# Kernel tuning notes

Hardware: AMD Instinct MI355X
Metric: run time of the kernel (lower is better)

## Reference

```python
import jax, jax.numpy as jnp
import numpy as np

NCLS, NDF, B = 256, 512, 1024
ALP = 0.1


def setup_inputs() -> dict:
    key = jax.random.key(0)
    k1, k2, k3 = jax.random.split(key, 3)
    df = jax.random.normal(k1, (B, NDF), dtype=jnp.float32)
    gt = jax.random.randint(k2, (B,), 0, NCLS)
    fc = jax.random.normal(k3, (NCLS, NDF), dtype=jnp.float32)
    return {"df": df, "gt": gt, "fc": fc}


def _update_stats(df, gt):
    """Sequential per-sample running mean/var update (moving_avg=False branch).
    Faithful to the torch no_grad loop: per-class counter `it`, c1=it/(it+1),
    c2=1/(it+1); mean[t]=f when it==0 else mean[t]*c1+f*c2;
    var[t]=var[t]*c1 + (f-mean[t])**2 * c1*c2. Buffers start at zero.
    """
    mean0 = jnp.zeros((NCLS, NDF), jnp.float32)
    var0 = jnp.zeros((NCLS, NDF), jnp.float32)
    it0 = jnp.zeros((NCLS,), jnp.int32)

    def step(carry, xt):
        mean, var, it = carry
        f, t = xt
        n = it[t]
        nf = n.astype(jnp.float32)
        c1 = nf / (nf + 1.0)
        c2 = 1.0 / (nf + 1.0)
        m_t = jnp.where(n == 0, f, mean[t] * c1 + f * c2)
        a = (f - m_t) ** 2
        v_t = var[t] * c1 + a * c1 * c2
        return (mean.at[t].set(m_t), var.at[t].set(v_t), it.at[t].add(1)), None

    (mean, var, it), _ = jax.lax.scan(step, (mean0, var0, it0), (df, gt))
    return mean, var


def reference(df, gt, fc):
    # stats updated from detached features (torch uses no_grad)
    _, var = _update_stats(jax.lax.stop_gradient(df), gt)
    Var = var[gt]          # (B, ndf)
    Fc = fc[gt]            # (B, ndf): column of fc for each sample's class
    W = fc[None, :, :] - Fc[:, None, :]  # (B, ncls, ndf)
    # score[b,c] = W[b,c,:].df[b,:] + alp/2 * (W**2)[b,c,:].Var[b,:]
    score = jnp.einsum('bcd,bd->bc', W, df) \
        + 0.5 * ALP * jnp.einsum('bcd,bd->bc', W * W, Var)
    return score[:, :, None]  # (B, ncls, 1), matching torch matmul output
```

## Files before the change

### kernel.cpp

```cpp
#include <hip/hip_runtime.h>

#define NCLS 256
#define NDF  512
#define BSZ  1024
#define ALP  0.1f


typedef __attribute__((ext_vector_type(8))) short bf16x8;
typedef __attribute__((ext_vector_type(4))) float f32x4;

__device__ __forceinline__ unsigned rne_pk(float lo, float hi) {
    union { float f; unsigned u; } a, b;
    a.f = lo; b.f = hi;
    unsigned ua = (a.u + 0x7FFFu + ((a.u >> 16) & 1u)) >> 16;
    unsigned ub = (b.u + 0x7FFFu + ((b.u >> 16) & 1u)) & 0xFFFF0000u;
    return ua | ub;
}
__device__ __forceinline__ uint4 pk16(float4 p, float4 q) {
    uint4 r;
    r.x = rne_pk(p.x, p.y); r.y = rne_pk(p.z, p.w);
    r.z = rne_pk(q.x, q.y); r.w = rne_pk(q.z, q.w);
    return r;
}
__device__ __forceinline__ float bf16r(float x) {
    union { float f; unsigned u; } c; c.f = x;
    c.u = (c.u + 0x7FFFu + ((c.u >> 16) & 1u)) & 0xFFFF0000u;
    return c.f;
}

__global__ __launch_bounds__(512) void k1_R_bias(const float* __restrict__ df,
                                                 const int* __restrict__ gt,
                                                 const float* __restrict__ fc,
                                                 float* __restrict__ Rp,
                                                 float* __restrict__ bias1) {
    __shared__ union {
        struct { alignas(16) char A[64 * 256]; alignas(16) char B[64 * 256]; } g;
        struct { int gts[BSZ]; unsigned long long bmap[64 * 16]; } r;
    } sm;

    const int tid = threadIdx.x;
    const int bid = blockIdx.x;
    const int lane = tid & 63;
    const int wv = tid >> 6;

    for (int i = tid; i < BSZ; i += 512) sm.r.gts[i] = gt[i];
    for (int i = tid; i < 1024; i += 512) sm.r.bmap[i] = 0ull;
    __syncthreads();
    for (int i = tid; i < BSZ; i += 512) {
        const int c = sm.r.gts[i] - ((bid >> 3) & 3) * 64;
        if ((unsigned)c < 64u) atomicOr(&sm.r.bmap[c * 16 + (i >> 6)], 1ull << (i & 63));
    }

    const int z = bid & 7;
    const int tile = bid >> 3;
    const int bm = tile & 3, bn = tile >> 2;
    const int D0 = z * 64;
    const int sr = tid >> 2;
    const int sswz = (sr & 7) << 4;
    const int clocal = sr;
    const int myclass = bm * 64 + (clocal & 63);
    const int dim0 = D0 + (tid & 3) * 16;
    const int kbl = (tid & 3) * 32;
    const int kbq = 128 + kbl;

    float fcq[16];
    float4 b0, b1, b2, b3;
    int bsample = 0, bt = 0;
    if (wv < 4) {
        const float* Bg = fc + (bn * 64 + sr) * NDF + dim0;
        b0 = ((const float4*)Bg)[0]; b1 = ((const float4*)Bg)[1];
        b2 = ((const float4*)Bg)[2]; b3 = ((const float4*)Bg)[3];
        const float* fct = fc + myclass * NDF + dim0;
        const float4 q0 = ((const float4*)fct)[0], q1 = ((const float4*)fct)[1];
        const float4 q2 = ((const float4*)fct)[2], q3 = ((const float4*)fct)[3];
        fcq[0]=q0.x; fcq[1]=q0.y; fcq[2]=q0.z; fcq[3]=q0.w;
        fcq[4]=q1.x; fcq[5]=q1.y; fcq[6]=q1.z; fcq[7]=q1.w;
        fcq[8]=q2.x; fcq[9]=q2.y; fcq[10]=q2.z; fcq[11]=q2.w;
        fcq[12]=q3.x; fcq[13]=q3.y; fcq[14]=q3.z; fcq[15]=q3.w;
    } else {
        bsample = bid * 8 + (wv - 4) * 2 + (lane >> 5);
        bt = sm.r.gts[bsample];
    }
    __syncthreads();

    float m[16], v[16];
    if (wv < 4) {
#pragma unroll
        for (int j = 0; j < 16; ++j) { m[j] = 0.f; v[j] = 0.f; }
        float nf = 0.f;
        int w = 0;
        unsigned long long bits = sm.r.bmap[clocal * 16];
        auto next = [&]() -> int {
            while (bits == 0ull) {
                if (w >= 15) return -1;
                bits = sm.r.bmap[clocal * 16 + (++w)];
            }
            const int b = __ffsll((unsigned long long)bits) - 1;
            bits &= bits - 1ull;
            return (w << 6) + b;
        };
        int cur = next();
        float f[16];
        if (cur >= 0) {
            const float* p = df + cur * NDF + dim0;
            const float4 q0 = ((const float4*)p)[0], q1 = ((const float4*)p)[1];
            const float4 q2 = ((const float4*)p)[2], q3 = ((const float4*)p)[3];
            f[0]=q0.x; f[1]=q0.y; f[2]=q0.z; f[3]=q0.w;
            f[4]=q1.x; f[5]=q1.y; f[6]=q1.z; f[7]=q1.w;
            f[8]=q2.x; f[9]=q2.y; f[10]=q2.z; f[11]=q2.w;
            f[12]=q3.x; f[13]=q3.y; f[14]=q3.z; f[15]=q3.w;
        }
        while (cur >= 0) {
            const int nxt = next();
            float g[16];
            if (nxt >= 0) {
                const float* p = df + nxt * NDF + dim0;
                const float4 q0 = ((const float4*)p)[0], q1 = ((const float4*)p)[1];
                const float4 q2 = ((const float4*)p)[2], q3 = ((const float4*)p)[3];
                g[0]=q0.x; g[1]=q0.y; g[2]=q0.z; g[3]=q0.w;
                g[4]=q1.x; g[5]=q1.y; g[6]=q1.z; g[7]=q1.w;
                g[8]=q2.x; g[9]=q2.y; g[10]=q2.z; g[11]=q2.w;
                g[12]=q3.x; g[13]=q3.y; g[14]=q3.z; g[15]=q3.w;
            }
            const float c2 = 1.0f / (nf + 1.0f);
            const float c1 = nf * c2;
            const float c12 = c1 * c2;
#pragma unroll
            for (int j = 0; j < 16; ++j) {
                m[j] = m[j] * c1 + f[j] * c2;
                const float a = f[j] - m[j];
                v[j] = v[j] * c1 + a * a * c12;
            }
            nf += 1.0f;
#pragma unroll
            for (int j = 0; j < 16; ++j) f[j] = g[j];
            cur = nxt;
        }
    } else {
        const int l32 = lane & 31;
        const float* pd = df + bsample * NDF + l32 * 16;
        const float* pf = fc + bt * NDF + l32 * 16;
        float s = 0.f;
#pragma unroll
        for (int i = 0; i < 4; ++i) {
            const float4 dq = ((const float4*)pd)[i];
            const float4 fq = ((const float4*)pf)[i];
            s = fmaf(bf16r(dq.x), bf16r(fq.x), s);
            s = fmaf(bf16r(dq.y), bf16r(fq.y), s);
            s = fmaf(bf16r(dq.z), bf16r(fq.z), s);
            s = fmaf(bf16r(dq.w), bf16r(fq.w), s);
        }
        s += __shfl_xor(s, 1); s += __shfl_xor(s, 2); s += __shfl_xor(s, 4);
        s += __shfl_xor(s, 8); s += __shfl_xor(s, 16);
        if (l32 == 0) bias1[bsample] = s;
    }
    __syncthreads();

    if (wv < 4) {
        char* arow = sm.g.A + sr * 256;
        char* brow = sm.g.B + sr * 256;
        float4 l0, l1, l2, l3;
        l0.x=-2.f*fcq[0]*v[0];  l0.y=-2.f*fcq[1]*v[1];  l0.z=-2.f*fcq[2]*v[2];  l0.w=-2.f*fcq[3]*v[3];
        l1.x=-2.f*fcq[4]*v[4];  l1.y=-2.f*fcq[5]*v[5];  l1.z=-2.f*fcq[6]*v[6];  l1.w=-2.f*fcq[7]*v[7];
        l2.x=-2.f*fcq[8]*v[8];  l2.y=-2.f*fcq[9]*v[9];  l2.z=-2.f*fcq[10]*v[10]; l2.w=-2.f*fcq[11]*v[11];
        l3.x=-2.f*fcq[12]*v[12]; l3.y=-2.f*fcq[13]*v[13]; l3.z=-2.f*fcq[14]*v[14]; l3.w=-2.f*fcq[15]*v[15];
        float4 p0, p1, p2, p3;
        p0.x=v[0];  p0.y=v[1];  p0.z=v[2];  p0.w=v[3];
        p1.x=v[4];  p1.y=v[5];  p1.z=v[6];  p1.w=v[7];
        p2.x=v[8];  p2.y=v[9];  p2.z=v[10]; p2.w=v[11];
        p3.x=v[12]; p3.y=v[13]; p3.z=v[14]; p3.w=v[15];
        float4 s0, s1, s2, s3;
        s0.x=b0.x*b0.x; s0.y=b0.y*b0.y; s0.z=b0.z*b0.z; s0.w=b0.w*b0.w;
        s1.x=b1.x*b1.x; s1.y=b1.y*b1.y; s1.z=b1.z*b1.z; s1.w=b1.w*b1.w;
        s2.x=b2.x*b2.x; s2.y=b2.y*b2.y; s2.z=b2.z*b2.z; s2.w=b2.w*b2.w;
        s3.x=b3.x*b3.x; s3.y=b3.y*b3.y; s3.z=b3.z*b3.z; s3.w=b3.w*b3.w;
        *(uint4*)(arow + ((kbl + 0) ^ sswz)) = pk16(l0, l1);
        *(uint4*)(arow + ((kbl + 16) ^ sswz)) = pk16(l2, l3);
        *(uint4*)(arow + ((kbq + 0) ^ sswz)) = pk16(p0, p1);
        *(uint4*)(arow + ((kbq + 16) ^ sswz)) = pk16(p2, p3);
        *(uint4*)(brow + ((kbl + 0) ^ sswz)) = pk16(b0, b1);
        *(uint4*)(brow + ((kbl + 16) ^ sswz)) = pk16(b2, b3);
        *(uint4*)(brow + ((kbq + 0) ^ sswz)) = pk16(s0, s1);
        *(uint4*)(brow + ((kbq + 16) ^ sswz)) = pk16(s2, s3);
    }
    __syncthreads();

    if (wv < 4) {
        const int fr = lane & 15;
        const int fkb = (lane >> 4) * 16;
        const int fswz = (fr & 7) << 4;
        const int wm = (wv >> 1) * 32, wn = (wv & 1) * 32;
        f32x4 acc[2][2];
        acc[0][0] = 0.f; acc[0][1] = 0.f; acc[1][0] = 0.f; acc[1][1] = 0.f;
#pragma unroll
        for (int st = 0; st < 4; ++st) {
            const int kb = (st * 64 + fkb) ^ fswz;
            const bf16x8 aF0 = *(const bf16x8*)(sm.g.A + (wm + fr) * 256 + kb);
            const bf16x8 aF1 = *(const bf16x8*)(sm.g.A + (wm + 16 + fr) * 256 + kb);
            const bf16x8 bF0 = *(const bf16x8*)(sm.g.B + (wn + fr) * 256 + kb);
            const bf16x8 bF1 = *(const bf16x8*)(sm.g.B + (wn + 16 + fr) * 256 + kb);
            acc[0][0] = __builtin_amdgcn_mfma_f32_16x16x32_bf16(aF0, bF0, acc[0][0], 0, 0, 0);
            acc[0][1] = __builtin_amdgcn_mfma_f32_16x16x32_bf16(aF0, bF1, acc[0][1], 0, 0, 0);
            acc[1][0] = __builtin_amdgcn_mfma_f32_16x16x32_bf16(aF1, bF0, acc[1][0], 0, 0, 0);
            acc[1][1] = __builtin_amdgcn_mfma_f32_16x16x32_bf16(aF1, bF1, acc[1][1], 0, 0, 0);
        }
        float* base = Rp + z * (NCLS * NCLS) + (bm * 64) * NCLS + bn * 64;
#pragma unroll
        for (int mi = 0; mi < 2; ++mi)
#pragma unroll
            for (int ni = 0; ni < 2; ++ni)
#pragma unroll
                for (int r2 = 0; r2 < 4; ++r2)
                    base[(wm + mi * 16 + (lane >> 4) * 4 + r2) * NCLS + wn + ni * 16 + fr] =
                        acc[mi][ni][r2];
    }
}

__global__ __launch_bounds__(512) void k2_s1_out(const float* __restrict__ df,
                                                 const int* __restrict__ gt,
                                                 const float* __restrict__ fc,
                                                 const float* __restrict__ Rp,
                                                 const float* __restrict__ bias1,
                                                 float* __restrict__ out) {
    __shared__ union {
        struct { alignas(16) char A[32 * 1024]; alignas(16) char B[32 * 1024]; } t;
        float fold[8 * 256];
    } sm;

    const int tid = threadIdx.x;
    const int bn = blockIdx.x & 7, bm = blockIdx.x >> 3;
    const int lane = tid & 63, wv = tid >> 6;

    const int row = tid >> 4, seg = tid & 15;
    const float* Ag = df + (bm * 32 + row) * NDF + seg * 32;
    const float* Bg = fc + (bn * 32 + row) * NDF + seg * 32;
    float4 a[8], b[8];
#pragma unroll
    for (int i = 0; i < 8; ++i) a[i] = ((const float4*)Ag)[i];
#pragma unroll
    for (int i = 0; i < 8; ++i) b[i] = ((const float4*)Bg)[i];
    const int swz = (row & 7) << 4;
    char* ar = sm.t.A + row * 1024;
    char* br = sm.t.B + row * 1024;
#pragma unroll
    for (int j = 0; j < 4; ++j)
        *(uint4*)(ar + ((seg * 64 + j * 16) ^ swz)) = pk16(a[2 * j], a[2 * j + 1]);
#pragma unroll
    for (int j = 0; j < 4; ++j)
        *(uint4*)(br + ((seg * 64 + j * 16) ^ swz)) = pk16(b[2 * j], b[2 * j + 1]);
    __syncthreads();

    const int q = wv & 3, h = wv >> 2;
    const int wm = (q >> 1) * 16, wn = (q & 1) * 16;
    const int fr = lane & 15;
    const int fkb = (lane >> 4) * 16;
    const int fswz = (fr & 7) << 4;
    f32x4 acc = 0.f;
#pragma unroll
    for (int s = 0; s < 8; ++s) {
        const int kb = ((h * 8 + s) * 64 + fkb) ^ fswz;
        const bf16x8 aF = *(const bf16x8*)(sm.t.A + (wm + fr) * 1024 + kb);
        const bf16x8 bF = *(const bf16x8*)(sm.t.B + (wn + fr) * 1024 + kb);
        acc = __builtin_amdgcn_mfma_f32_16x16x32_bf16(aF, bF, acc, 0, 0, 0);
    }
    __syncthreads();
    ((f32x4*)sm.fold)[wv * 64 + lane] = acc;
    __syncthreads();
    const f32x4 other = ((f32x4*)sm.fold)[(wv ^ 4) * 64 + lane];
    acc += other;

    const int colg = bn * 32 + wn + fr;
#pragma unroll
    for (int rr = 0; rr < 2; ++rr) {
        const float av = h ? ((rr == 0) ? acc[2] : acc[3])
                           : ((rr == 0) ? acc[0] : acc[1]);
        const int r = h * 2 + rr;
        const int bg = bm * 32 + wm + (lane >> 4) * 4 + r;
        const int t = gt[bg];
        float vR = 0.f, vtt = 0.f;
#pragma unroll
        for (int z = 0; z < 8; ++z) {
            const float* rp = Rp + z * (NCLS * NCLS) + t * NCLS;
            vR += rp[colg];
            vtt += rp[t];
        }
        out[bg * NCLS + colg] = (av - bias1[bg]) + 0.5f * ALP * (vR - vtt);
    }
}

extern "C" void kernel_launch(void* const* d_in, const int* in_sizes, int n_in,
                              void* d_out, int out_size, void* d_ws, size_t ws_size,
                              hipStream_t stream) {
    const float* df = (const float*)d_in[0];
    const int* gt = (const int*)d_in[1];
    const float* fc = (const float*)d_in[2];
    float* out = (float*)d_out;

    float* ws = (float*)d_ws;
    float* Rp = ws;
    float* bias1 = Rp + 8 * NCLS * NCLS;

    k1_R_bias<<<128, 512, 0, stream>>>(df, gt, fc, Rp, bias1);
    k2_s1_out<<<256, 512, 0, stream>>>(df, gt, fc, Rp, bias1, out);
}
```

Measured before the change: 25.34 us.

## Load MFMA fragments directly from global in k2, drop LDS staging and K-split

The second kernel no longer stages df/fc tiles through swizzled LDS. Each lane now loads its bf16 fragments straight from global memory and packs them in registers. The K-split across two wave halves, with its LDS fold and barriers, is replaced by 4 waves that each cover the full K using two interleaved accumulators, and the block size drops from 512 to 256 threads. This removes LDS traffic and three syncthreads, but each element is now loaded redundantly by the waves sharing a row or column, and each wave runs a longer serial MFMA chain.

```diff
diff --git a/kernel.cpp b/kernel.cpp
--- a/kernel.cpp
+++ b/kernel.cpp
@@ -21,6 +21,9 @@
     r.x = rne_pk(p.x, p.y); r.y = rne_pk(p.z, p.w);
     r.z = rne_pk(q.x, q.y); r.w = rne_pk(q.z, q.w);
     return r;
+}
+__device__ __forceinline__ bf16x8 pkfrag(float4 p, float4 q) {
+    return __builtin_bit_cast(bf16x8, pk16(p, q));
 }
 __device__ __forceinline__ float bf16r(float x) {
     union { float f; unsigned u; } c; c.f = x;
@@ -216,65 +219,40 @@
     }
 }
 
-__global__ __launch_bounds__(512) void k2_s1_out(const float* __restrict__ df,
+__global__ __launch_bounds__(256) void k2_s1_out(const float* __restrict__ df,
                                                  const int* __restrict__ gt,
                                                  const float* __restrict__ fc,
                                                  const float* __restrict__ Rp,
                                                  const float* __restrict__ bias1,
                                                  float* __restrict__ out) {
-    __shared__ union {
-        struct { alignas(16) char A[32 * 1024]; alignas(16) char B[32 * 1024]; } t;
-        float fold[8 * 256];
-    } sm;
-
     const int tid = threadIdx.x;
     const int bn = blockIdx.x & 7, bm = blockIdx.x >> 3;
     const int lane = tid & 63, wv = tid >> 6;
-
-    const int row = tid >> 4, seg = tid & 15;
-    const float* Ag = df + (bm * 32 + row) * NDF + seg * 32;
-    const float* Bg = fc + (bn * 32 + row) * NDF + seg * 32;
-    float4 a[8], b[8];
-#pragma unroll
-    for (int i = 0; i < 8; ++i) a[i] = ((const float4*)Ag)[i];
-#pragma unroll
-    for (int i = 0; i < 8; ++i) b[i] = ((const float4*)Bg)[i];
-    const int swz = (row & 7) << 4;
-    char* ar = sm.t.A + row * 1024;
-    char* br = sm.t.B + row * 1024;
-#pragma unroll
-    for (int j = 0; j < 4; ++j)
-        *(uint4*)(ar + ((seg * 64 + j * 16) ^ swz)) = pk16(a[2 * j], a[2 * j + 1]);
-#pragma unroll
-    for (int j = 0; j < 4; ++j)
-        *(uint4*)(br + ((seg * 64 + j * 16) ^ swz)) = pk16(b[2 * j], b[2 * j + 1]);
-    __syncthreads();
-
-    const int q = wv & 3, h = wv >> 2;
-    const int wm = (q >> 1) * 16, wn = (q & 1) * 16;
+    const int wm = (wv >> 1) * 16, wn = (wv & 1) * 16;
     const int fr = lane & 15;
-    const int fkb = (lane >> 4) * 16;
-    const int fswz = (fr & 7) << 4;
-    f32x4 acc = 0.f;
-#pragma unroll
-    for (int s = 0; s < 8; ++s) {
-        const int kb = ((h * 8 + s) * 64 + fkb) ^ fswz;
-        const bf16x8 aF = *(const bf16x8*)(sm.t.A + (wm + fr) * 1024 + kb);
-        const bf16x8 bF = *(const bf16x8*)(sm.t.B + (wn + fr) * 1024 + kb);
-        acc = __builtin_amdgcn_mfma_f32_16x16x32_bf16(aF, bF, acc, 0, 0, 0);
-    }
-    __syncthreads();
-    ((f32x4*)sm.fold)[wv * 64 + lane] = acc;
-    __syncthreads();
-    const f32x4 other = ((f32x4*)sm.fold)[(wv ^ 4) * 64 + lane];
-    acc += other;
+    const int ksub = (lane >> 4) * 8;
+
+    const float* Arow = df + (bm * 32 + wm + fr) * NDF + ksub;
+    const float* Brow = fc + (bn * 32 + wn + fr) * NDF + ksub;
+
+    f32x4 accE = 0.f, accO = 0.f;
+#pragma unroll
+    for (int s = 0; s < 16; s += 2) {
+        const float4 a00 = ((const float4*)(Arow + s * 32))[0];
+        const float4 a01 = ((const float4*)(Arow + s * 32))[1];
+        const float4 b00 = ((const float4*)(Brow + s * 32))[0];
+        const float4 b01 = ((const float4*)(Brow + s * 32))[1];
+        const float4 a10 = ((const float4*)(Arow + s * 32 + 32))[0];
+        const float4 a11 = ((const float4*)(Arow + s * 32 + 32))[1];
+        const float4 b10 = ((const float4*)(Brow + s * 32 + 32))[0];
+        const float4 b11 = ((const float4*)(Brow + s * 32 + 32))[1];
+        accE = __builtin_amdgcn_mfma_f32_16x16x32_bf16(pkfrag(a00, a01), pkfrag(b00, b01), accE, 0, 0, 0);
+        accO = __builtin_amdgcn_mfma_f32_16x16x32_bf16(pkfrag(a10, a11), pkfrag(b10, b11), accO, 0, 0, 0);
+    }
 
     const int colg = bn * 32 + wn + fr;
 #pragma unroll
-    for (int rr = 0; rr < 2; ++rr) {
-        const float av = h ? ((rr == 0) ? acc[2] : acc[3])
-                           : ((rr == 0) ? acc[0] : acc[1]);
-        const int r = h * 2 + rr;
+    for (int r = 0; r < 4; ++r) {
         const int bg = bm * 32 + wm + (lane >> 4) * 4 + r;
         const int t = gt[bg];
         float vR = 0.f, vtt = 0.f;
@@ -284,7 +262,8 @@
             vR += rp[colg];
             vtt += rp[t];
         }
-        out[bg * NCLS + colg] = (av - bias1[bg]) + 0.5f * ALP * (vR - vtt);
+        out[bg * NCLS + colg] = (accE[r] + accO[r] - bias1[bg])
+                                + 0.5f * ALP * (vR - vtt);
     }
 }
 
@@ -301,5 +280,5 @@
     float* bias1 = Rp + 8 * NCLS * NCLS;
 
     k1_R_bias<<<128, 512, 0, stream>>>(df, gt, fc, Rp, bias1);
-    k2_s1_out<<<256, 512, 0, stream>>>(df, gt, fc, Rp, bias1, out);
-}
+    k2_s1_out<<<256, 256, 0, stream>>>(df, gt, fc, Rp, bias1, out);
+}
```

Result: slower. 35.04 us (+38.3%).
